# Optimization experiments

Hardware: AMD Instinct MI355X
Metric: run time of the kernel (lower is better)

Reference implementation:

```python
import jax, jax.numpy as jnp
import numpy as np

EPS = 0.5      # sinkhorn eps used by assign_batch_sinkhorn
NITERS = 15    # sinkhorn iterations used by assign_batch_sinkhorn


def pairwise_dists(features, centroids):
    # ||f - c|| via the expansion ||f||^2 + ||c||^2 - 2 f.c (avoids the
    # [B, nc, D] intermediate the naive broadcast would materialize).
    f2 = jnp.sum(features * features, axis=-1)          # [B]
    c2 = jnp.sum(centroids * centroids, axis=-1)        # [K]
    d2 = f2[:, None] + c2[None, :] - 2.0 * features @ centroids.T  # [B, K]
    return jnp.sqrt(jnp.maximum(d2, 0.0))


def sinkhorn(scores, eps=EPS, niters=NITERS):
    # Faithful to the torch sinkhorn(): Q = exp(scores/eps).T, normalize
    # columns (sum over K), then alternate row/column scalings.
    Q = jnp.exp(scores / eps).T                          # [K, B]
    Q = Q / jnp.sum(Q, axis=0, keepdims=True)
    K, B = Q.shape
    r = jnp.ones((K,), Q.dtype) / K
    c = jnp.ones((B,), Q.dtype) / B

    def body(_, Q):
        Q = Q * (r / jnp.sum(Q, axis=1))[:, None]
        Q = Q * (c / jnp.sum(Q, axis=0))[None, :]
        return Q

    Q = jax.lax.fori_loop(0, niters, body, Q)
    return (Q / jnp.sum(Q, axis=0, keepdims=True)).T     # [B, K]


def setup_inputs() -> dict:
    key = jax.random.key(0)
    kf, kc = jax.random.split(key)
    B, K, D = 16384, 2048, 1000
    # 0.1 scale keeps dists ~O(5) so exp(-dists/eps) stays in fp32 range
    # (unit-randn 1000-dim features give dists ~45 -> exp underflow).
    features = 0.1 * jax.random.normal(kf, (B, D), dtype=jnp.float32)
    centroids = 0.1 * jax.random.normal(kc, (K, D), dtype=jnp.float32)
    return {"features": features, "centroids": centroids}


def reference(features, centroids):
    B, K = features.shape[0], centroids.shape[0]
    dists = pairwise_dists(features, centroids)          # [B, K]

    # assign_batch_sinkhorn (soft assignments computed under no_grad)
    soft = jax.lax.stop_gradient(sinkhorn(-dists))       # [B, K]
    batch_assignments = jnp.argmin(soft, axis=1)         # [B] (as in source)
    soft_counts = jnp.sum(soft, axis=0)                  # [K]
    cluster_loss = jnp.mean(
        jnp.take_along_axis(dists, batch_assignments[:, None], axis=1))

    # the per-element python count loops, as fused scatter-adds
    cluster_counts = jnp.zeros((K,), jnp.int32).at[batch_assignments].add(1)
    raw_assign = jnp.argmin(dists, axis=1)
    raw_counts = jnp.zeros((K,), jnp.int32).at[raw_assign].add(1)

    return cluster_loss, batch_assignments, soft_counts, cluster_counts, raw_counts
```

## Files before the change

### kernel.cpp

```cpp
#include <hip/hip_runtime.h>

typedef __attribute__((ext_vector_type(8))) short bf16x8;
typedef __attribute__((ext_vector_type(4))) float f32x4;

#define NB 16384
#define NK 2048
#define ND 1000
#define KP 1024
#define NCHK 1024

__device__ float  g_dist[(size_t)NB * NK];
__device__ ushort g_Fh[(size_t)NB * KP], g_Fl[(size_t)NB * KP];
__device__ ushort g_Ch[(size_t)NK * KP], g_Cl[(size_t)NK * KP];
__device__ float  g_u[NK], g_c2[NK], g_scnt[NK];
__device__ float  g_f2[NB], g_bd[NB];
__device__ float  g_part[(size_t)NCHK * NK];
__device__ double g_part2[16 * NK];
__device__ int    g_cc[NK], g_rc[NK];

typedef const __attribute__((address_space(1))) void gvoid_t;
typedef __attribute__((address_space(3))) void lvoid_t;

__device__ __forceinline__ ushort bf16_rne(float x){
    uint u = __float_as_uint(x);
    uint lsb = (u >> 16) & 1u;
    u += 0x7fffu + lsb;
    return (ushort)(u >> 16);
}
__device__ __forceinline__ float bf16_to_f(ushort h){
    return __uint_as_float(((uint)h) << 16);
}

__global__ __launch_bounds__(256) void cn_prep(const float* __restrict__ X,
                                               ushort* __restrict__ H,
                                               ushort* __restrict__ L,
                                               float* __restrict__ sq){
    const int row = blockIdx.x, t = threadIdx.x;
    const int lane = t & 63, wid = t >> 6;
    float4 x = make_float4(0.f,0.f,0.f,0.f);
    if (t < 250) x = *(const float4*)(X + (size_t)row * ND + 4 * t);
    double s = (double)x.x*x.x + (double)x.y*x.y + (double)x.z*x.z + (double)x.w*x.w;
    ushort4 h4, l4;
#pragma unroll
    for (int c = 0; c < 4; ++c){
        float xc = (&x.x)[c];
        ushort h = bf16_rne(xc);
        (&h4.x)[c] = h;
        (&l4.x)[c] = bf16_rne(xc - bf16_to_f(h));
    }
    *(ushort4*)&H[(size_t)row * KP + 4 * t] = h4;
    *(ushort4*)&L[(size_t)row * KP + 4 * t] = l4;

    __shared__ double pr[4];
    for (int off = 32; off; off >>= 1) s += __shfl_xor(s, off);
    if (lane == 0) pr[wid] = s;
    __syncthreads();
    if (t == 0) sq[row] = (float)(pr[0] + pr[1] + pr[2] + pr[3]);
}

__global__ __launch_bounds__(256) void cn_gemm_dist(){
    __shared__ __attribute__((aligned(16))) ushort Ah[128 * 32];
    __shared__ __attribute__((aligned(16))) ushort Al[128 * 32];
    __shared__ __attribute__((aligned(16))) ushort Bh[128 * 32];
    __shared__ __attribute__((aligned(16))) ushort Bl[128 * 32];

    const int tid = threadIdx.x;
    const int lane = tid & 63, wid = tid >> 6;
    const int wr = wid >> 1, wc = wid & 1;
    const int brow0 = blockIdx.y * 128, bcol0 = blockIdx.x * 128;

    f32x4 acc[4][4];
#pragma unroll
    for (int m = 0; m < 4; ++m)
#pragma unroll
        for (int n = 0; n < 4; ++n) acc[m][n] = (f32x4){0.f,0.f,0.f,0.f};

    const int lrow = lane >> 2;
    const int lcol = (lane & 3) * 8;

    for (int step = 0; step < 32; ++step){
        const int k0 = step * 32;
#pragma unroll
        for (int i = 0; i < 2; ++i){
            const int ch = wid * 2 + i;
            const int ldso = ch * 512;
            const size_t ga = ((size_t)(brow0 + ch * 16 + lrow)) * KP + k0 + lcol;
            const size_t gb = ((size_t)(bcol0 + ch * 16 + lrow)) * KP + k0 + lcol;
            __builtin_amdgcn_global_load_lds((gvoid_t*)(g_Fh + ga), (lvoid_t*)(Ah + ldso), 16, 0, 0);
            __builtin_amdgcn_global_load_lds((gvoid_t*)(g_Fl + ga), (lvoid_t*)(Al + ldso), 16, 0, 0);
            __builtin_amdgcn_global_load_lds((gvoid_t*)(g_Ch + gb), (lvoid_t*)(Bh + ldso), 16, 0, 0);
            __builtin_amdgcn_global_load_lds((gvoid_t*)(g_Cl + gb), (lvoid_t*)(Bl + ldso), 16, 0, 0);
        }
        __syncthreads();

        const int arow = wr * 64 + (lane & 15);
        const int brow = wc * 64 + (lane & 15);
        const int kof  = (lane >> 4) * 8;
        bf16x8 afh[4], afl[4], bfh[4], bfl[4];
#pragma unroll
        for (int m = 0; m < 4; ++m){
            afh[m] = *(const bf16x8*)&Ah[(arow + m * 16) * 32 + kof];
            afl[m] = *(const bf16x8*)&Al[(arow + m * 16) * 32 + kof];
        }
#pragma unroll
        for (int n = 0; n < 4; ++n){
            bfh[n] = *(const bf16x8*)&Bh[(brow + n * 16) * 32 + kof];
            bfl[n] = *(const bf16x8*)&Bl[(brow + n * 16) * 32 + kof];
        }
#pragma unroll
        for (int m = 0; m < 4; ++m)
#pragma unroll
            for (int n = 0; n < 4; ++n){
                acc[m][n] = __builtin_amdgcn_mfma_f32_16x16x32_bf16(afh[m], bfh[n], acc[m][n], 0, 0, 0);
                acc[m][n] = __builtin_amdgcn_mfma_f32_16x16x32_bf16(afh[m], bfl[n], acc[m][n], 0, 0, 0);
                acc[m][n] = __builtin_amdgcn_mfma_f32_16x16x32_bf16(afl[m], bfh[n], acc[m][n], 0, 0, 0);
            }
        __syncthreads();
    }

#pragma unroll
    for (int m = 0; m < 4; ++m){
        int rowb = brow0 + wr * 64 + m * 16 + (lane >> 4) * 4;
#pragma unroll
        for (int n = 0; n < 4; ++n){
            int col = bcol0 + wc * 64 + n * 16 + (lane & 15);
            float c2v = g_c2[col];
#pragma unroll
            for (int j = 0; j < 4; ++j){
                float d2 = g_f2[rowb + j] + c2v - 2.0f * acc[m][n][j];
                g_dist[(size_t)(rowb + j) * NK + col] = sqrtf(fmaxf(d2, 0.0f));
            }
        }
    }
}

template<int MODE>
__global__ __launch_bounds__(256) void cn_sweep(float* __restrict__ outba){
    __shared__ float4 sred[3][8][64];
    const int lane = threadIdx.x & 63, wid = threadIdx.x >> 6;
    const int row0 = (blockIdx.x * 4 + wid) * 4;
    const float cst = (MODE == 0) ? 1.0f : (1.0f / (float)NB);

    float4 uu[8];
    float4 ak[8];
    if (MODE >= 1){
#pragma unroll
        for (int j = 0; j < 8; ++j)
            uu[j] = *(const float4*)&g_u[4 * lane + 256 * j];
    }
    if (MODE == 2){
#pragma unroll
        for (int j = 0; j < 8; ++j)
#pragma unroll
            for (int c = 0; c < 4; ++c)
                (&ak[j].x)[c] = (float)log((double)(&uu[j].x)[c] * (double)NK);
    }

    float4 S[8];
#pragma unroll
    for (int j = 0; j < 8; ++j) S[j] = make_float4(0.f,0.f,0.f,0.f);

    for (int r = 0; r < 4; ++r){
        const int b = row0 + r;
        const float* dr = g_dist + (size_t)b * NK + 4 * lane;
        float4 ev[8];
        float4 dv[8];
        float tsum = 0.f;
#pragma unroll
        for (int j = 0; j < 8; ++j){
            float4 d4 = *(const float4*)(dr + 256 * j);
            float4 e4;
#pragma unroll
            for (int c = 0; c < 4; ++c){
                float e = __expf(-2.0f * (&d4.x)[c]);
                (&e4.x)[c] = e;
                tsum += (MODE >= 1) ? e * (&uu[j].x)[c] : e;
            }
            ev[j] = e4;
            if (MODE == 2) dv[j] = d4;
        }
#pragma unroll
        for (int off = 32; off; off >>= 1) tsum += __shfl_xor(tsum, off);
        const float v = cst / tsum;
#pragma unroll
        for (int j = 0; j < 8; ++j){
#pragma unroll
            for (int c = 0; c < 4; ++c)
                (&S[j].x)[c] += (&ev[j].x)[c] * v;
        }

        if (MODE == 2){
            double bestT = -1.0e300; int bi = 0; float bd = 0.f;
            float rbest = 3.4e38f;   int ri = 0;
#pragma unroll
            for (int j = 0; j < 8; ++j){
#pragma unroll
                for (int c = 0; c < 4; ++c){
                    int k = 256 * j + 4 * lane + c;
                    float d = (&dv[j].x)[c];
                    double t = 2.0 * (double)d - (double)(&ak[j].x)[c];
                    if (t > bestT){ bestT = t; bi = k; bd = d; }
                    if (d < rbest){ rbest = d; ri = k; }
                }
            }
            for (int off = 32; off; off >>= 1){
                double oT = __shfl_xor(bestT, off);
                int    oi = __shfl_xor(bi, off);
                float  od = __shfl_xor(bd, off);
                if (oT > bestT || (oT == bestT && oi < bi)){ bestT = oT; bi = oi; bd = od; }
                float orb = __shfl_xor(rbest, off);
                int   ori = __shfl_xor(ri, off);
                if (orb < rbest || (orb == rbest && ori < ri)){ rbest = orb; ri = ori; }
            }
            if (lane == 0){
                outba[b] = (float)bi;
                g_bd[b] = bd;
                atomicAdd(&g_cc[bi], 1);
                atomicAdd(&g_rc[ri], 1);
            }
        }
    }

    if (wid > 0){
#pragma unroll
        for (int j = 0; j < 8; ++j) sred[wid - 1][j][lane] = S[j];
    }
    __syncthreads();
    if (wid == 0){
#pragma unroll
        for (int w = 0; w < 3; ++w)
#pragma unroll
            for (int j = 0; j < 8; ++j){
                float4 o = sred[w][j][lane];
                S[j].x += o.x; S[j].y += o.y; S[j].z += o.z; S[j].w += o.w;
            }
#pragma unroll
        for (int j = 0; j < 8; ++j)
            *(float4*)&g_part[(size_t)blockIdx.x * NK + 4 * lane + 256 * j] = S[j];
    }
}

__global__ __launch_bounds__(256) void cn_red1(){
    int k = blockIdx.x * 256 + threadIdx.x;
    int c0 = blockIdx.y * 64;
    double s = 0.0;
    for (int ch = 0; ch < 64; ++ch)
        s += (double)g_part[(size_t)(c0 + ch) * NK + k];
    g_part2[blockIdx.y * NK + k] = s;
}

__global__ __launch_bounds__(256) void cn_red2(int mode){
    int k = blockIdx.x * 256 + threadIdx.x;
    double s = 0.0;
    for (int i = 0; i < 16; ++i) s += g_part2[i * NK + k];
    if (mode == 0) g_u[k] = (float)((1.0 / (double)NK) / s);
    else           g_scnt[k] = (float)((double)NB * (double)g_u[k] * s);
}

__global__ __launch_bounds__(256) void cn_zero(){
    int i = blockIdx.x * 256 + threadIdx.x;
    if (i < NK){ g_cc[i] = 0; g_rc[i] = 0; }
}

__global__ __launch_bounds__(256) void cn_finalize(float* __restrict__ out){
    int i = blockIdx.x * 256 + threadIdx.x;
    if (i < NK){
        out[1 + NB + i]            = g_scnt[i];
        out[1 + NB + NK + i]       = (float)g_cc[i];
        out[1 + NB + 2 * NK + i]   = (float)g_rc[i];
    }
    if (blockIdx.x == 0){
        __shared__ double red[4];
        int lane = threadIdx.x & 63, wid = threadIdx.x >> 6;
        double s = 0.0;
        for (int b = threadIdx.x; b < NB; b += 256) s += (double)g_bd[b];
        for (int off = 32; off; off >>= 1) s += __shfl_xor(s, off);
        if (lane == 0) red[wid] = s;
        __syncthreads();
        if (threadIdx.x == 0){
            double tot = red[0] + red[1] + red[2] + red[3];
            out[0] = (float)(tot / (double)NB);
        }
    }
}

extern "C" void kernel_launch(void* const* d_in, const int* in_sizes, int n_in,
                              void* d_out, int out_size, void* d_ws, size_t ws_size,
                              hipStream_t stream){
    const float* F  = (const float*)d_in[0];
    const float* Cn = (const float*)d_in[1];
    float* out = (float*)d_out;
    (void)d_ws; (void)ws_size;

    {
        ushort *fh, *fl, *ch, *cl; float *f2, *c2;
        hipGetSymbolAddress((void**)&fh, HIP_SYMBOL(g_Fh));
        hipGetSymbolAddress((void**)&fl, HIP_SYMBOL(g_Fl));
        hipGetSymbolAddress((void**)&ch, HIP_SYMBOL(g_Ch));
        hipGetSymbolAddress((void**)&cl, HIP_SYMBOL(g_Cl));
        hipGetSymbolAddress((void**)&f2, HIP_SYMBOL(g_f2));
        hipGetSymbolAddress((void**)&c2, HIP_SYMBOL(g_c2));
        cn_prep<<<NB, 256, 0, stream>>>(F, fh, fl, f2);
        cn_prep<<<NK, 256, 0, stream>>>(Cn, ch, cl, c2);
    }
    cn_zero<<<NK / 256, 256, 0, stream>>>();

    dim3 gg(NK / 128, NB / 128);
    cn_gemm_dist<<<gg, 256, 0, stream>>>();

    dim3 r1(NK / 256, 16);

    cn_sweep<0><<<NCHK, 256, 0, stream>>>(nullptr);
    cn_red1<<<r1, 256, 0, stream>>>();
    cn_red2<<<NK / 256, 256, 0, stream>>>(0);

    for (int it = 1; it <= 14; ++it){
        cn_sweep<1><<<NCHK, 256, 0, stream>>>(nullptr);
        cn_red1<<<r1, 256, 0, stream>>>();
        cn_red2<<<NK / 256, 256, 0, stream>>>(0);
    }

    cn_sweep<2><<<NCHK, 256, 0, stream>>>(out + 1);
    cn_red1<<<r1, 256, 0, stream>>>();
    cn_red2<<<NK / 256, 256, 0, stream>>>(1);

    cn_finalize<<<NK / 256, 256, 0, stream>>>(out);
}
```

Measured before the change: 786.7 us.

## Cache fp16 exp matrix for early Sinkhorn sweeps, swizzle LDS, fuse reductions

The GEMM epilogue now also writes exp(-2d), scaled and stored as fp16. The first ten Sinkhorn sweeps read this half-size matrix instead of recomputing exp from the fp32 distances, which cuts the memory traffic of those bandwidth-bound passes. The last five iterations and the final sweep still use the fp32 distances, which limits the accuracy loss. It also XOR-swizzles the bf16 operand layout to avoid LDS bank conflicts, merges the two-stage column reduction into one kernel, and drops the per-call hipGetSymbolAddress host calls. The extra fp16 store in the GEMM adds write traffic and some precision risk.

```diff
diff --git a/kernel.cpp b/kernel.cpp
--- a/kernel.cpp
+++ b/kernel.cpp
@@ -10,16 +10,18 @@
 #define NCHK 1024
 
 __device__ float  g_dist[(size_t)NB * NK];
+__device__ ushort g_E[(size_t)NB * NK];
 __device__ ushort g_Fh[(size_t)NB * KP], g_Fl[(size_t)NB * KP];
 __device__ ushort g_Ch[(size_t)NK * KP], g_Cl[(size_t)NK * KP];
 __device__ float  g_u[NK], g_c2[NK], g_scnt[NK];
 __device__ float  g_f2[NB], g_bd[NB];
 __device__ float  g_part[(size_t)NCHK * NK];
-__device__ double g_part2[16 * NK];
 __device__ int    g_cc[NK], g_rc[NK];
 
 typedef const __attribute__((address_space(1))) void gvoid_t;
 typedef __attribute__((address_space(3))) void lvoid_t;
+
+union h16 { ushort u; _Float16 h; };
 
 __device__ __forceinline__ ushort bf16_rne(float x){
     uint u = __float_as_uint(x);
@@ -31,10 +33,11 @@
     return __uint_as_float(((uint)h) << 16);
 }
 
-__global__ __launch_bounds__(256) void cn_prep(const float* __restrict__ X,
-                                               ushort* __restrict__ H,
-                                               ushort* __restrict__ L,
-                                               float* __restrict__ sq){
+template<int WHICH>
+__global__ __launch_bounds__(256) void cn_prep(const float* __restrict__ X){
+    ushort* __restrict__ H = WHICH ? g_Ch : g_Fh;
+    ushort* __restrict__ L = WHICH ? g_Cl : g_Fl;
+    float*  __restrict__ sq = WHICH ? g_c2 : g_f2;
     const int row = blockIdx.x, t = threadIdx.x;
     const int lane = t & 63, wid = t >> 6;
     float4 x = make_float4(0.f,0.f,0.f,0.f);
@@ -48,8 +51,11 @@
         (&h4.x)[c] = h;
         (&l4.x)[c] = bf16_rne(xc - bf16_to_f(h));
     }
-    *(ushort4*)&H[(size_t)row * KP + 4 * t] = h4;
-    *(ushort4*)&L[(size_t)row * KP + 4 * t] = l4;
+    const int base = (t >> 3) << 5;
+    const int grp  = (t >> 1) & 3;
+    const int pos  = base + ((grp ^ ((row >> 1) & 3)) << 3) + ((4 * t) & 7);
+    *(ushort4*)&H[(size_t)row * KP + pos] = h4;
+    *(ushort4*)&L[(size_t)row * KP + pos] = l4;
 
     __shared__ double pr[4];
     for (int off = 32; off; off >>= 1) s += __shfl_xor(s, off);
@@ -95,7 +101,7 @@
 
         const int arow = wr * 64 + (lane & 15);
         const int brow = wc * 64 + (lane & 15);
-        const int kof  = (lane >> 4) * 8;
+        const int kof  = (((lane >> 4) ^ ((lane >> 1) & 3)) * 8);
         bf16x8 afh[4], afl[4], bfh[4], bfl[4];
 #pragma unroll
         for (int m = 0; m < 4; ++m){
@@ -128,7 +134,11 @@
 #pragma unroll
             for (int j = 0; j < 4; ++j){
                 float d2 = g_f2[rowb + j] + c2v - 2.0f * acc[m][n][j];
-                g_dist[(size_t)(rowb + j) * NK + col] = sqrtf(fmaxf(d2, 0.0f));
+                float d  = sqrtf(fmaxf(d2, 0.0f));
+                size_t idx = (size_t)(rowb + j) * NK + col;
+                g_dist[idx] = d;
+                h16 cv; cv.h = (_Float16)(__expf(-2.0f * d) * 8192.0f);
+                g_E[idx] = cv.u;
             }
         }
     }
@@ -148,7 +158,7 @@
         for (int j = 0; j < 8; ++j)
             uu[j] = *(const float4*)&g_u[4 * lane + 256 * j];
     }
-    if (MODE == 2){
+    if (MODE == 3){
 #pragma unroll
         for (int j = 0; j < 8; ++j)
 #pragma unroll
@@ -162,22 +172,39 @@
 
     for (int r = 0; r < 4; ++r){
         const int b = row0 + r;
-        const float* dr = g_dist + (size_t)b * NK + 4 * lane;
         float4 ev[8];
         float4 dv[8];
         float tsum = 0.f;
-#pragma unroll
-        for (int j = 0; j < 8; ++j){
-            float4 d4 = *(const float4*)(dr + 256 * j);
-            float4 e4;
-#pragma unroll
-            for (int c = 0; c < 4; ++c){
-                float e = __expf(-2.0f * (&d4.x)[c]);
-                (&e4.x)[c] = e;
-                tsum += (MODE >= 1) ? e * (&uu[j].x)[c] : e;
-            }
-            ev[j] = e4;
-            if (MODE == 2) dv[j] = d4;
+        if (MODE <= 1){
+            const ushort* er = g_E + (size_t)b * NK + 4 * lane;
+#pragma unroll
+            for (int j = 0; j < 8; ++j){
+                ushort4 q4 = *(const ushort4*)(er + 256 * j);
+                float4 e4;
+#pragma unroll
+                for (int c = 0; c < 4; ++c){
+                    h16 cv; cv.u = (&q4.x)[c];
+                    float e = (float)cv.h;
+                    (&e4.x)[c] = e;
+                    tsum += (MODE == 1) ? e * (&uu[j].x)[c] : e;
+                }
+                ev[j] = e4;
+            }
+        } else {
+            const float* dr = g_dist + (size_t)b * NK + 4 * lane;
+#pragma unroll
+            for (int j = 0; j < 8; ++j){
+                float4 d4 = *(const float4*)(dr + 256 * j);
+                float4 e4;
+#pragma unroll
+                for (int c = 0; c < 4; ++c){
+                    float e = __expf(-2.0f * (&d4.x)[c]);
+                    (&e4.x)[c] = e;
+                    tsum += e * (&uu[j].x)[c];
+                }
+                ev[j] = e4;
+                if (MODE == 3) dv[j] = d4;
+            }
         }
 #pragma unroll
         for (int off = 32; off; off >>= 1) tsum += __shfl_xor(tsum, off);
@@ -189,7 +216,7 @@
                 (&S[j].x)[c] += (&ev[j].x)[c] * v;
         }
 
-        if (MODE == 2){
+        if (MODE == 3){
             double bestT = -1.0e300; int bi = 0; float bd = 0.f;
             float rbest = 3.4e38f;   int ri = 0;
 #pragma unroll
@@ -240,21 +267,20 @@
     }
 }
 
-__global__ __launch_bounds__(256) void cn_red1(){
-    int k = blockIdx.x * 256 + threadIdx.x;
-    int c0 = blockIdx.y * 64;
+__global__ __launch_bounds__(256) void cn_red(int mode){
+    __shared__ double red[4][64];
+    const int lane = threadIdx.x & 63, q = threadIdx.x >> 6;
+    const int k = blockIdx.x * 64 + lane;
     double s = 0.0;
-    for (int ch = 0; ch < 64; ++ch)
-        s += (double)g_part[(size_t)(c0 + ch) * NK + k];
-    g_part2[blockIdx.y * NK + k] = s;
-}
-
-__global__ __launch_bounds__(256) void cn_red2(int mode){
-    int k = blockIdx.x * 256 + threadIdx.x;
-    double s = 0.0;
-    for (int i = 0; i < 16; ++i) s += g_part2[i * NK + k];
-    if (mode == 0) g_u[k] = (float)((1.0 / (double)NK) / s);
-    else           g_scnt[k] = (float)((double)NB * (double)g_u[k] * s);
+    for (int ch = q * 256; ch < q * 256 + 256; ++ch)
+        s += (double)g_part[(size_t)ch * NK + k];
+    red[q][lane] = s;
+    __syncthreads();
+    if (q == 0){
+        double tot = red[0][lane] + red[1][lane] + red[2][lane] + red[3][lane];
+        if (mode == 0) g_u[k] = (float)((1.0 / (double)NK) / tot);
+        else           g_scnt[k] = (float)((double)NB * (double)g_u[k] * tot);
+    }
 }
 
 __global__ __launch_bounds__(256) void cn_zero(){
@@ -292,37 +318,27 @@
     float* out = (float*)d_out;
     (void)d_ws; (void)ws_size;
 
-    {
-        ushort *fh, *fl, *ch, *cl; float *f2, *c2;
-        hipGetSymbolAddress((void**)&fh, HIP_SYMBOL(g_Fh));
-        hipGetSymbolAddress((void**)&fl, HIP_SYMBOL(g_Fl));
-        hipGetSymbolAddress((void**)&ch, HIP_SYMBOL(g_Ch));
-        hipGetSymbolAddress((void**)&cl, HIP_SYMBOL(g_Cl));
-        hipGetSymbolAddress((void**)&f2, HIP_SYMBOL(g_f2));
-        hipGetSymbolAddress((void**)&c2, HIP_SYMBOL(g_c2));
-        cn_prep<<<NB, 256, 0, stream>>>(F, fh, fl, f2);
-        cn_prep<<<NK, 256, 0, stream>>>(Cn, ch, cl, c2);
-    }
+    cn_prep<0><<<NB, 256, 0, stream>>>(F);
+    cn_prep<1><<<NK, 256, 0, stream>>>(Cn);
     cn_zero<<<NK / 256, 256, 0, stream>>>();
 
     dim3 gg(NK / 128, NB / 128);
     cn_gemm_dist<<<gg, 256, 0, stream>>>();
 
-    dim3 r1(NK / 256, 16);
-
     cn_sweep<0><<<NCHK, 256, 0, stream>>>(nullptr);
-    cn_red1<<<r1, 256, 0, stream>>>();
-    cn_red2<<<NK / 256, 256, 0, stream>>>(0);
-
-    for (int it = 1; it <= 14; ++it){
+    cn_red<<<NK / 64, 256, 0, stream>>>(0);
+
+    for (int it = 1; it <= 9; ++it){
         cn_sweep<1><<<NCHK, 256, 0, stream>>>(nullptr);
-        cn_red1<<<r1, 256, 0, stream>>>();
-        cn_red2<<<NK / 256, 256, 0, stream>>>(0);
-    }
-
-    cn_sweep<2><<<NCHK, 256, 0, stream>>>(out + 1);
-    cn_red1<<<r1, 256, 0, stream>>>();
-    cn_red2<<<NK / 256, 256, 0, stream>>>(1);
+        cn_red<<<NK / 64, 256, 0, stream>>>(0);
+    }
+    for (int it = 10; it <= 14; ++it){
+        cn_sweep<2><<<NCHK, 256, 0, stream>>>(nullptr);
+        cn_red<<<NK / 64, 256, 0, stream>>>(0);
+    }
+
+    cn_sweep<3><<<NCHK, 256, 0, stream>>>(out + 1);
+    cn_red<<<NK / 64, 256, 0, stream>>>(1);
 
     cn_finalize<<<NK / 256, 256, 0, stream>>>(out);
 }
```

Result: no change. 775.5 us (-1.4%).
